# Kernel tuning notes

Measured on AMD Instinct MI355X. Metric: run time of the kernel, lower is better.

The kernel has to match this reference:

```python
import jax, jax.numpy as jnp
import numpy as np

N = 100000      # nodes
E = 3200000     # edges (avg degree 32)
F = 256         # input features
C = 256         # output channels


def setup_inputs() -> dict:
    key = jax.random.key(0)
    k1, k2, k3, k4, k5 = jax.random.split(key, 5)
    x = jax.random.normal(k1, (N, F), dtype=jnp.float32)
    edge_row = jax.random.randint(k2, (E,), 0, N, dtype=jnp.int32)
    edge_col = jax.random.randint(k3, (E,), 0, N, dtype=jnp.int32)
    # precomputed normalized adjacency values (D^-1/2 (A+I) D^-1/2 entries)
    edge_vals = jax.random.uniform(k4, (E,), dtype=jnp.float32)
    kernel = jax.random.normal(k5, (F, C), dtype=jnp.float32) * (1.0 / np.sqrt(F))
    bias = jnp.zeros((C,), dtype=jnp.float32)
    return {"x": x, "edge_row": edge_row, "edge_col": edge_col,
            "edge_vals": edge_vals, "kernel": kernel, "bias": bias}


def reference(x, edge_row, edge_col, edge_vals, kernel, bias):
    # GraphConv: Z = relu( A_hat @ (X @ W) + b ), single mode, sparse A_hat.
    h = x @ kernel                                   # [N, C]
    msgs = edge_vals[:, None] * h[edge_col]          # [E, C] gather along cols
    agg = jax.ops.segment_sum(msgs, edge_row, num_segments=N)  # [N, C]
    return jax.nn.relu(agg + bias)
```

## Files before the change

kernel.cpp:

```cpp
#include <hip/hip_runtime.h>
#include <hip/hip_bf16.h>
#include <hip/hip_fp16.h>


#define BROWS 128
#define CH_A1 16384
#define CH_A3 8192
#define GEMM_SMEM 10240

typedef __attribute__((ext_vector_type(4))) float f32x4;
typedef __attribute__((ext_vector_type(8))) short s16x8;

__device__ __forceinline__ unsigned short f2bf(float f) {
    unsigned u = __float_as_uint(f);
    u += 0x7FFFu + ((u >> 16) & 1u);
    return (unsigned short)(u >> 16);
}
__device__ __forceinline__ float bf2f(unsigned short s) {
    return __uint_as_float(((unsigned)s) << 16);
}

__global__ __launch_bounds__(256) void k_wt(const float* __restrict__ W,
                                            unsigned short* __restrict__ Wt) {
    int idx = blockIdx.x * 256 + threadIdx.x;
    int k = idx >> 8, c = idx & 255;
    Wt[c * 256 + k] = f2bf(W[idx]);
}

__device__ __forceinline__ void gemm_body(const float* __restrict__ X,
                                          const unsigned short* __restrict__ Wt,
                                          unsigned short* __restrict__ H,
                                          int M, int g, char* smem) {
    typedef unsigned short AsRow[40];
    AsRow* As = (AsRow*)smem;
    int t = threadIdx.x;
    int lane = t & 63;
    int w = t >> 6;
    int wm = w & 1, wn = w >> 1;
    int rb = g >> 2, cb4 = g & 3;
    int r0 = rb * 128, c0 = cb4 * 64;

    int srow = t >> 2;
    int sslot = t & 3;
    int gr0 = r0 + srow;        if (gr0 >= M) gr0 = M - 1;
    int gr1 = r0 + 64 + srow;   if (gr1 >= M) gr1 = M - 1;

    f32x4 acc[4][2] = {};

    for (int k0 = 0; k0 < 256; k0 += 32) {
        const float* p0 = &X[(size_t)gr0 * 256 + k0 + sslot * 8];
        const float* p1 = &X[(size_t)gr1 * 256 + k0 + sslot * 8];
        float4 a0 = *(const float4*)p0;
        float4 a1 = *(const float4*)(p0 + 4);
        float4 b0 = *(const float4*)p1;
        float4 b1 = *(const float4*)(p1 + 4);
        s16x8 va, vb;
        va[0] = (short)f2bf(a0.x); va[1] = (short)f2bf(a0.y);
        va[2] = (short)f2bf(a0.z); va[3] = (short)f2bf(a0.w);
        va[4] = (short)f2bf(a1.x); va[5] = (short)f2bf(a1.y);
        va[6] = (short)f2bf(a1.z); va[7] = (short)f2bf(a1.w);
        vb[0] = (short)f2bf(b0.x); vb[1] = (short)f2bf(b0.y);
        vb[2] = (short)f2bf(b0.z); vb[3] = (short)f2bf(b0.w);
        vb[4] = (short)f2bf(b1.x); vb[5] = (short)f2bf(b1.y);
        vb[6] = (short)f2bf(b1.z); vb[7] = (short)f2bf(b1.w);
        __syncthreads();
        *(s16x8*)&As[srow][sslot * 8] = va;
        *(s16x8*)&As[srow + 64][sslot * 8] = vb;
        __syncthreads();

        int kofs = (lane >> 4) * 8;
        s16x8 afr[4], bfr[2];
#pragma unroll
        for (int mi = 0; mi < 4; ++mi)
            afr[mi] = *(const s16x8*)&As[wm * 64 + mi * 16 + (lane & 15)][kofs];
#pragma unroll
        for (int ni = 0; ni < 2; ++ni) {
            int cn = c0 + wn * 32 + ni * 16 + (lane & 15);
            bfr[ni] = *(const s16x8*)&Wt[(size_t)cn * 256 + k0 + kofs];
        }
#pragma unroll
        for (int mi = 0; mi < 4; ++mi)
#pragma unroll
            for (int ni = 0; ni < 2; ++ni)
                acc[mi][ni] = __builtin_amdgcn_mfma_f32_16x16x32_bf16(
                    afr[mi], bfr[ni], acc[mi][ni], 0, 0, 0);
    }

#pragma unroll
    for (int mi = 0; mi < 4; ++mi) {
#pragma unroll
        for (int ni = 0; ni < 2; ++ni) {
            int rg = r0 + wm * 64 + mi * 16 + (lane >> 4) * 4;
            int cg = c0 + wn * 32 + ni * 16 + (lane & 15);
#pragma unroll
            for (int j = 0; j < 4; ++j) {
                if (rg + j < M)
                    H[(size_t)(rg + j) * 256 + cg] = f2bf(acc[mi][ni][j]);
            }
        }
    }
}

__device__ __forceinline__ void hist_body(const int* __restrict__ row,
                                          int* __restrict__ gcnt,
                                          int E, int NB, int chunk, char* smem) {
    int* h = (int*)smem;
    int t = threadIdx.x;
    for (int j = t; j < NB; j += 256) h[j] = 0;
    __syncthreads();
    int start = chunk * CH_A1;
    int end = min(E, start + CH_A1);
    for (int i = start + t; i < end; i += 256)
        atomicAdd(&h[row[i] >> 7], 1);
    __syncthreads();
    for (int j = t; j < NB; j += 256)
        if (h[j]) atomicAdd(&gcnt[j], h[j]);
}

__device__ __forceinline__ void a3_body(const int* __restrict__ row,
                                        const int* __restrict__ col,
                                        const float* __restrict__ val,
                                        int* __restrict__ gcur,
                                        int2* __restrict__ binned,
                                        int E, int NB, int chunk, char* smem) {
    int* h    = (int*)smem;
    int* base = h + NB;
    int* cur  = base + NB;
    int t = threadIdx.x;
    for (int j = t; j < NB; j += 256) { h[j] = 0; cur[j] = 0; }
    __syncthreads();
    int start = chunk * CH_A3;
    int end = min(E, start + CH_A3);
    for (int i = start + t; i < end; i += 256)
        atomicAdd(&h[row[i] >> 7], 1);
    __syncthreads();
    for (int j = t; j < NB; j += 256) {
        int c = h[j];
        base[j] = c ? atomicAdd(&gcur[j], c) : 0;
    }
    __syncthreads();
    for (int i = start + t; i < end; i += 256) {
        int r = row[i];
        int b = r >> 7;
        int ofs = atomicAdd(&cur[b], 1);
        unsigned hb = (unsigned)__half_as_ushort(__float2half(val[i]));
        binned[base[b] + ofs] = make_int2(col[i] | (int)(hb << 17), r & (BROWS - 1));
    }
}

__device__ __forceinline__ void kb_body(const int2* __restrict__ binned,
                                        const int* __restrict__ bkt_base,
                                        int* __restrict__ rowptr,
                                        unsigned* __restrict__ csr,
                                        int N, int b, char* smem) {
    int* cnt = (int*)smem;
    int* sc  = cnt + BROWS;
    int* cur = sc + BROWS;
    int t = threadIdx.x;
    int r0 = b * BROWS;
    int bb = bkt_base[b];
    int be = bkt_base[b + 1];
    if (t < BROWS) cnt[t] = 0;
    __syncthreads();
    for (int i = bb + t; i < be; i += 256)
        atomicAdd(&cnt[binned[i].y], 1);
    __syncthreads();
    if (t < BROWS) sc[t] = cnt[t];
    __syncthreads();
    for (int off = 1; off < BROWS; off <<= 1) {
        int tmp = (t < BROWS && t >= off) ? sc[t - off] : 0;
        __syncthreads();
        if (t < BROWS && t >= off) sc[t] += tmp;
        __syncthreads();
    }
    if (t < BROWS) {
        int ex = sc[t] - cnt[t];
        cur[t] = ex;
        if (r0 + t < N) rowptr[r0 + t] = bb + ex;
    }
    __syncthreads();
    for (int i = bb + t; i < be; i += 256) {
        int2 e = binned[i];
        int ofs = atomicAdd(&cur[e.y], 1);
        csr[bb + ofs] = (unsigned)e.x;
    }
}

__global__ __launch_bounds__(1024) void kA2(const int* __restrict__ gcnt,
                                            int* __restrict__ bkt_base,
                                            int* __restrict__ gcur,
                                            int* __restrict__ rowptr,
                                            int NB, int N, int E) {
    __shared__ int s[1024];
    int t = threadIdx.x;
    int v = (t < NB) ? gcnt[t] : 0;
    s[t] = v;
    __syncthreads();
    for (int off = 1; off < 1024; off <<= 1) {
        int tmp = (t >= off) ? s[t - off] : 0;
        __syncthreads();
        if (t >= off) s[t] += tmp;
        __syncthreads();
    }
    if (t < NB) {
        int ex = s[t] - v;
        bkt_base[t] = ex;
        gcur[t] = ex;
    }
    if (t == 0) {
        bkt_base[NB] = E;
        rowptr[N] = E;
    }
}

__global__ __launch_bounds__(256) void h0(const int* __restrict__ row,
                                          int* __restrict__ gcnt,
                                          int E, int NB, int nHist,
                                          const float* __restrict__ X,
                                          const unsigned short* __restrict__ Wt,
                                          unsigned short* __restrict__ H,
                                          int M, int g0) {
    extern __shared__ char smem[];
    int bid = blockIdx.x;
    if (bid < nHist) { hist_body(row, gcnt, E, NB, bid, smem); return; }
    gemm_body(X, Wt, H, M, g0 + (bid - nHist), smem);
}

__global__ __launch_bounds__(256) void h1(const int* __restrict__ row,
                                          const int* __restrict__ col,
                                          const float* __restrict__ val,
                                          int* __restrict__ gcur,
                                          int2* __restrict__ binned,
                                          int E, int NB, int nA3,
                                          const float* __restrict__ X,
                                          const unsigned short* __restrict__ Wt,
                                          unsigned short* __restrict__ H,
                                          int M, int g0) {
    extern __shared__ char smem[];
    int bid = blockIdx.x;
    if (bid < nA3) { a3_body(row, col, val, gcur, binned, E, NB, bid, smem); return; }
    gemm_body(X, Wt, H, M, g0 + (bid - nA3), smem);
}

__global__ __launch_bounds__(256) void h2(const int2* __restrict__ binned,
                                          const int* __restrict__ bktb,
                                          int* __restrict__ rowptr,
                                          unsigned* __restrict__ csr,
                                          int N, int NB,
                                          const float* __restrict__ X,
                                          const unsigned short* __restrict__ Wt,
                                          unsigned short* __restrict__ H,
                                          int M, int g0) {
    extern __shared__ char smem[];
    int bid = blockIdx.x;
    if (bid < NB) { kb_body(binned, bktb, rowptr, csr, N, bid, smem); return; }
    gemm_body(X, Wt, H, M, g0 + (bid - NB), smem);
}

__global__ __launch_bounds__(256) void k_gemm_solo(const float* __restrict__ X,
                                                   const unsigned short* __restrict__ Wt,
                                                   unsigned short* __restrict__ H, int M) {
    extern __shared__ char smem[];
    gemm_body(X, Wt, H, M, blockIdx.x, smem);
}

__global__ __launch_bounds__(256) void k_agg(const unsigned short* __restrict__ H,
                                             const int* __restrict__ rowptr,
                                             const unsigned* __restrict__ csr,
                                             const float* __restrict__ bias,
                                             float* __restrict__ out, int n) {
    int wave = threadIdx.x >> 6;
    int lane = threadIdx.x & 63;
    int node = blockIdx.x * 4 + wave;
    if (node >= n) return;
    int s = rowptr[node];
    int e = rowptr[node + 1];
    int h = lane >> 5;
    int cbase = (lane & 31) * 8;

    float a0=0.f,a1=0.f,a2=0.f,a3=0.f,a4=0.f,a5=0.f,a6=0.f,a7=0.f;

#define ACC(K, HV)                                                      \
    {                                                                   \
        float v = __half2float(__ushort_as_half((unsigned short)((K) >> 17))); \
        a0 += v * bf2f((unsigned short)(HV)[0]);                        \
        a1 += v * bf2f((unsigned short)(HV)[1]);                        \
        a2 += v * bf2f((unsigned short)(HV)[2]);                        \
        a3 += v * bf2f((unsigned short)(HV)[3]);                        \
        a4 += v * bf2f((unsigned short)(HV)[4]);                        \
        a5 += v * bf2f((unsigned short)(HV)[5]);                        \
        a6 += v * bf2f((unsigned short)(HV)[6]);                        \
        a7 += v * bf2f((unsigned short)(HV)[7]);                        \
    }

    int i = s;
    for (; i + 11 < e; i += 12) {
        unsigned k0 = csr[i + h];
        unsigned k1 = csr[i + 2 + h];
        unsigned k2 = csr[i + 4 + h];
        unsigned k3 = csr[i + 6 + h];
        unsigned k4 = csr[i + 8 + h];
        unsigned k5 = csr[i + 10 + h];
        s16x8 g0 = *(const s16x8*)&H[(k0 & 0x1FFFFu) * 256 + cbase];
        s16x8 g1 = *(const s16x8*)&H[(k1 & 0x1FFFFu) * 256 + cbase];
        s16x8 g2 = *(const s16x8*)&H[(k2 & 0x1FFFFu) * 256 + cbase];
        s16x8 g3 = *(const s16x8*)&H[(k3 & 0x1FFFFu) * 256 + cbase];
        s16x8 g4 = *(const s16x8*)&H[(k4 & 0x1FFFFu) * 256 + cbase];
        s16x8 g5 = *(const s16x8*)&H[(k5 & 0x1FFFFu) * 256 + cbase];
        ACC(k0, g0); ACC(k1, g1); ACC(k2, g2);
        ACC(k3, g3); ACC(k4, g4); ACC(k5, g5);
    }
    for (; i + 3 < e; i += 4) {
        unsigned k0 = csr[i + h];
        unsigned k1 = csr[i + 2 + h];
        s16x8 g0 = *(const s16x8*)&H[(k0 & 0x1FFFFu) * 256 + cbase];
        s16x8 g1 = *(const s16x8*)&H[(k1 & 0x1FFFFu) * 256 + cbase];
        ACC(k0, g0); ACC(k1, g1);
    }
    for (; i + 1 < e; i += 2) {
        unsigned k0 = csr[i + h];
        s16x8 g0 = *(const s16x8*)&H[(k0 & 0x1FFFFu) * 256 + cbase];
        ACC(k0, g0);
    }
    if (i < e) {
        unsigned k0 = csr[i];
        s16x8 g0 = *(const s16x8*)&H[(k0 & 0x1FFFFu) * 256 + cbase];
        float v = h ? 0.f
                    : __half2float(__ushort_as_half((unsigned short)(k0 >> 17)));
        a0 += v * bf2f((unsigned short)g0[0]);
        a1 += v * bf2f((unsigned short)g0[1]);
        a2 += v * bf2f((unsigned short)g0[2]);
        a3 += v * bf2f((unsigned short)g0[3]);
        a4 += v * bf2f((unsigned short)g0[4]);
        a5 += v * bf2f((unsigned short)g0[5]);
        a6 += v * bf2f((unsigned short)g0[6]);
        a7 += v * bf2f((unsigned short)g0[7]);
    }
#undef ACC

    a0 += __shfl_xor(a0, 32); a1 += __shfl_xor(a1, 32);
    a2 += __shfl_xor(a2, 32); a3 += __shfl_xor(a3, 32);
    a4 += __shfl_xor(a4, 32); a5 += __shfl_xor(a5, 32);
    a6 += __shfl_xor(a6, 32); a7 += __shfl_xor(a7, 32);

    float w0 = h ? a4 : a0;
    float w1 = h ? a5 : a1;
    float w2 = h ? a6 : a2;
    float w3 = h ? a7 : a3;
    int cw = cbase + h * 4;
    float4 b4 = *(const float4*)&bias[cw];
    float4 o;
    o.x = fmaxf(w0 + b4.x, 0.f);
    o.y = fmaxf(w1 + b4.y, 0.f);
    o.z = fmaxf(w2 + b4.z, 0.f);
    o.w = fmaxf(w3 + b4.w, 0.f);
    *(float4*)&out[node * 256 + cw] = o;
}

extern "C" void kernel_launch(void* const* d_in, const int* in_sizes, int n_in,
                              void* d_out, int out_size, void* d_ws, size_t ws_size,
                              hipStream_t stream) {
    const float* x     = (const float*)d_in[0];
    const int*   erow  = (const int*)d_in[1];
    const int*   ecol  = (const int*)d_in[2];
    const float* evals = (const float*)d_in[3];
    const float* W     = (const float*)d_in[4];
    const float* bias  = (const float*)d_in[5];
    float* out = (float*)d_out;

    const int C = 256;
    const int N = in_sizes[0] / C;
    const int E = in_sizes[1];
    const int NB = (N + BROWS - 1) / BROWS;

    char* ws = (char*)d_ws;
    size_t off = 0;
    auto carve = [&](size_t bytes) -> void* {
        void* p = ws + off;
        off += (bytes + 255) & ~(size_t)255;
        return p;
    };
    unsigned short* Hbf  = (unsigned short*)carve((size_t)N * C * 2);
    unsigned*       csr  = (unsigned*)carve((size_t)E * 4);
    int*            rowp = (int*)carve((size_t)(N + 1) * 4);
    unsigned short* Wt   = (unsigned short*)carve((size_t)C * 256 * 2);
    int*            gcnt = (int*)carve((size_t)NB * 4);
    int*            gcur = (int*)carve((size_t)NB * 4);
    int*            bktb = (int*)carve((size_t)(NB + 1) * 4);

    bool fused = (off + (size_t)E * 8) <= ws_size;
    int2* binned = fused ? (int2*)carve((size_t)E * 8) : (int2*)Hbf;

    int nHist = (E + CH_A1 - 1) / CH_A1;
    int nA3   = (E + CH_A3 - 1) / CH_A3;
    int gemmBlocks = ((N + 127) / 128) * 4;

    int G0 = fused ? 600 : 0;
    int G1 = fused ? 1400 : 0;
    int G2 = fused ? (gemmBlocks - 600 - 1400) : 0;

    hipMemsetAsync(gcnt, 0, (size_t)NB * 4, stream);
    k_wt<<<256, 256, 0, stream>>>(W, Wt);
    h0<<<nHist + G0, 256, GEMM_SMEM, stream>>>(erow, gcnt, E, NB, nHist,
                                               x, Wt, Hbf, N, 0);
    kA2<<<1, 1024, 0, stream>>>(gcnt, bktb, gcur, rowp, NB, N, E);
    h1<<<nA3 + G1, 256, GEMM_SMEM, stream>>>(erow, ecol, evals, gcur, binned,
                                             E, NB, nA3, x, Wt, Hbf, N, G0);
    h2<<<NB + G2, 256, GEMM_SMEM, stream>>>(binned, bktb, rowp, csr, N, NB,
                                            x, Wt, Hbf, N, G0 + G1);
    if (!fused)
        k_gemm_solo<<<gemmBlocks, 256, GEMM_SMEM, stream>>>(x, Wt, Hbf, N);

    k_agg<<<(N + 3) / 4, 256, 0, stream>>>(Hbf, rowp, csr, bias, out, N);
}
```

Before: 432.0 us.

## Retile GEMM to 64x256 blocks, fold weight transpose into histogram launch, use nontemporal accesses

The GEMM block tile changes from 128x64 to 64 rows by all 256 columns, so each X row is loaded and converted to bf16 once instead of four times. The weight transpose moves into the histogram kernel h0, and the GEMM blocks are redistributed across h1 and h2 only. Nontemporal loads and stores are added for X, the binned edges and the output. The aggregation unroll drops from 12 to 8 edges per iteration. The trade-off is more accumulator registers per wave and a different overlap balance between graph preprocessing and the GEMM.

```diff
diff --git a/kernel.cpp b/kernel.cpp
--- a/kernel.cpp
+++ b/kernel.cpp
@@ -9,6 +9,7 @@
 #define GEMM_SMEM 10240
 
 typedef __attribute__((ext_vector_type(4))) float f32x4;
+typedef __attribute__((ext_vector_type(2))) int i32x2;
 typedef __attribute__((ext_vector_type(8))) short s16x8;
 
 __device__ __forceinline__ unsigned short f2bf(float f) {
@@ -18,13 +19,6 @@
 }
 __device__ __forceinline__ float bf2f(unsigned short s) {
     return __uint_as_float(((unsigned)s) << 16);
-}
-
-__global__ __launch_bounds__(256) void k_wt(const float* __restrict__ W,
-                                            unsigned short* __restrict__ Wt) {
-    int idx = blockIdx.x * 256 + threadIdx.x;
-    int k = idx >> 8, c = idx & 255;
-    Wt[c * 256 + k] = f2bf(W[idx]);
 }
 
 __device__ __forceinline__ void gemm_body(const float* __restrict__ X,
@@ -36,52 +30,41 @@
     int t = threadIdx.x;
     int lane = t & 63;
     int w = t >> 6;
-    int wm = w & 1, wn = w >> 1;
-    int rb = g >> 2, cb4 = g & 3;
-    int r0 = rb * 128, c0 = cb4 * 64;
-
+    int r0 = g * 64;
+    int c0 = w * 64;
     int srow = t >> 2;
     int sslot = t & 3;
-    int gr0 = r0 + srow;        if (gr0 >= M) gr0 = M - 1;
-    int gr1 = r0 + 64 + srow;   if (gr1 >= M) gr1 = M - 1;
-
-    f32x4 acc[4][2] = {};
+    int gr = r0 + srow; if (gr >= M) gr = M - 1;
+
+    f32x4 acc[4][4] = {};
 
     for (int k0 = 0; k0 < 256; k0 += 32) {
-        const float* p0 = &X[(size_t)gr0 * 256 + k0 + sslot * 8];
-        const float* p1 = &X[(size_t)gr1 * 256 + k0 + sslot * 8];
-        float4 a0 = *(const float4*)p0;
-        float4 a1 = *(const float4*)(p0 + 4);
-        float4 b0 = *(const float4*)p1;
-        float4 b1 = *(const float4*)(p1 + 4);
-        s16x8 va, vb;
-        va[0] = (short)f2bf(a0.x); va[1] = (short)f2bf(a0.y);
-        va[2] = (short)f2bf(a0.z); va[3] = (short)f2bf(a0.w);
-        va[4] = (short)f2bf(a1.x); va[5] = (short)f2bf(a1.y);
-        va[6] = (short)f2bf(a1.z); va[7] = (short)f2bf(a1.w);
-        vb[0] = (short)f2bf(b0.x); vb[1] = (short)f2bf(b0.y);
-        vb[2] = (short)f2bf(b0.z); vb[3] = (short)f2bf(b0.w);
-        vb[4] = (short)f2bf(b1.x); vb[5] = (short)f2bf(b1.y);
-        vb[6] = (short)f2bf(b1.z); vb[7] = (short)f2bf(b1.w);
+        const float* p = &X[(size_t)gr * 256 + k0 + sslot * 8];
+        f32x4 a0 = __builtin_nontemporal_load((const f32x4*)p);
+        f32x4 a1 = __builtin_nontemporal_load((const f32x4*)(p + 4));
+        s16x8 va;
+        va[0] = (short)f2bf(a0[0]); va[1] = (short)f2bf(a0[1]);
+        va[2] = (short)f2bf(a0[2]); va[3] = (short)f2bf(a0[3]);
+        va[4] = (short)f2bf(a1[0]); va[5] = (short)f2bf(a1[1]);
+        va[6] = (short)f2bf(a1[2]); va[7] = (short)f2bf(a1[3]);
         __syncthreads();
         *(s16x8*)&As[srow][sslot * 8] = va;
-        *(s16x8*)&As[srow + 64][sslot * 8] = vb;
         __syncthreads();
 
         int kofs = (lane >> 4) * 8;
-        s16x8 afr[4], bfr[2];
+        s16x8 afr[4], bfr[4];
 #pragma unroll
         for (int mi = 0; mi < 4; ++mi)
-            afr[mi] = *(const s16x8*)&As[wm * 64 + mi * 16 + (lane & 15)][kofs];
-#pragma unroll
-        for (int ni = 0; ni < 2; ++ni) {
-            int cn = c0 + wn * 32 + ni * 16 + (lane & 15);
+            afr[mi] = *(const s16x8*)&As[mi * 16 + (lane & 15)][kofs];
+#pragma unroll
+        for (int ni = 0; ni < 4; ++ni) {
+            int cn = c0 + ni * 16 + (lane & 15);
             bfr[ni] = *(const s16x8*)&Wt[(size_t)cn * 256 + k0 + kofs];
         }
 #pragma unroll
         for (int mi = 0; mi < 4; ++mi)
 #pragma unroll
-            for (int ni = 0; ni < 2; ++ni)
+            for (int ni = 0; ni < 4; ++ni)
                 acc[mi][ni] = __builtin_amdgcn_mfma_f32_16x16x32_bf16(
                     afr[mi], bfr[ni], acc[mi][ni], 0, 0, 0);
     }
@@ -89,9 +72,9 @@
 #pragma unroll
     for (int mi = 0; mi < 4; ++mi) {
 #pragma unroll
-        for (int ni = 0; ni < 2; ++ni) {
-            int rg = r0 + wm * 64 + mi * 16 + (lane >> 4) * 4;
-            int cg = c0 + wn * 32 + ni * 16 + (lane & 15);
+        for (int ni = 0; ni < 4; ++ni) {
+            int rg = r0 + mi * 16 + (lane >> 4) * 4;
+            int cg = c0 + ni * 16 + (lane & 15);
 #pragma unroll
             for (int j = 0; j < 4; ++j) {
                 if (rg + j < M)
@@ -162,8 +145,10 @@
     int be = bkt_base[b + 1];
     if (t < BROWS) cnt[t] = 0;
     __syncthreads();
-    for (int i = bb + t; i < be; i += 256)
-        atomicAdd(&cnt[binned[i].y], 1);
+    for (int i = bb + t; i < be; i += 256) {
+        i32x2 e = __builtin_nontemporal_load((const i32x2*)&binned[i]);
+        atomicAdd(&cnt[e[1]], 1);
+    }
     __syncthreads();
     if (t < BROWS) sc[t] = cnt[t];
     __syncthreads();
@@ -180,9 +165,9 @@
     }
     __syncthreads();
     for (int i = bb + t; i < be; i += 256) {
-        int2 e = binned[i];
-        int ofs = atomicAdd(&cur[e.y], 1);
-        csr[bb + ofs] = (unsigned)e.x;
+        i32x2 e = __builtin_nontemporal_load((const i32x2*)&binned[i]);
+        int ofs = atomicAdd(&cur[e[1]], 1);
+        csr[bb + ofs] = (unsigned)e[0];
     }
 }
 
@@ -216,14 +201,15 @@
 __global__ __launch_bounds__(256) void h0(const int* __restrict__ row,
                                           int* __restrict__ gcnt,
                                           int E, int NB, int nHist,
-                                          const float* __restrict__ X,
-                                          const unsigned short* __restrict__ Wt,
-                                          unsigned short* __restrict__ H,
-                                          int M, int g0) {
+                                          const float* __restrict__ W,
+                                          unsigned short* __restrict__ Wt) {
     extern __shared__ char smem[];
     int bid = blockIdx.x;
+    int t = threadIdx.x;
     if (bid < nHist) { hist_body(row, gcnt, E, NB, bid, smem); return; }
-    gemm_body(X, Wt, H, M, g0 + (bid - nHist), smem);
+    int idx = (bid - nHist) * 256 + t;
+    int k = idx >> 8, c = idx & 255;
+    Wt[c * 256 + k] = f2bf(W[idx]);
 }
 
 __global__ __launch_bounds__(256) void h1(const int* __restrict__ row,
@@ -294,28 +280,16 @@
     }
 
     int i = s;
-    for (; i + 11 < e; i += 12) {
+    for (; i + 7 < e; i += 8) {
         unsigned k0 = csr[i + h];
         unsigned k1 = csr[i + 2 + h];
         unsigned k2 = csr[i + 4 + h];
         unsigned k3 = csr[i + 6 + h];
-        unsigned k4 = csr[i + 8 + h];
-        unsigned k5 = csr[i + 10 + h];
         s16x8 g0 = *(const s16x8*)&H[(k0 & 0x1FFFFu) * 256 + cbase];
         s16x8 g1 = *(const s16x8*)&H[(k1 & 0x1FFFFu) * 256 + cbase];
         s16x8 g2 = *(const s16x8*)&H[(k2 & 0x1FFFFu) * 256 + cbase];
         s16x8 g3 = *(const s16x8*)&H[(k3 & 0x1FFFFu) * 256 + cbase];
-        s16x8 g4 = *(const s16x8*)&H[(k4 & 0x1FFFFu) * 256 + cbase];
-        s16x8 g5 = *(const s16x8*)&H[(k5 & 0x1FFFFu) * 256 + cbase];
-        ACC(k0, g0); ACC(k1, g1); ACC(k2, g2);
-        ACC(k3, g3); ACC(k4, g4); ACC(k5, g5);
-    }
-    for (; i + 3 < e; i += 4) {
-        unsigned k0 = csr[i + h];
-        unsigned k1 = csr[i + 2 + h];
-        s16x8 g0 = *(const s16x8*)&H[(k0 & 0x1FFFFu) * 256 + cbase];
-        s16x8 g1 = *(const s16x8*)&H[(k1 & 0x1FFFFu) * 256 + cbase];
-        ACC(k0, g0); ACC(k1, g1);
+        ACC(k0, g0); ACC(k1, g1); ACC(k2, g2); ACC(k3, g3);
     }
     for (; i + 1 < e; i += 2) {
         unsigned k0 = csr[i + h];
@@ -349,12 +323,12 @@
     float w3 = h ? a7 : a3;
     int cw = cbase + h * 4;
     float4 b4 = *(const float4*)&bias[cw];
-    float4 o;
-    o.x = fmaxf(w0 + b4.x, 0.f);
-    o.y = fmaxf(w1 + b4.y, 0.f);
-    o.z = fmaxf(w2 + b4.z, 0.f);
-    o.w = fmaxf(w3 + b4.w, 0.f);
-    *(float4*)&out[node * 256 + cw] = o;
+    f32x4 o;
+    o[0] = fmaxf(w0 + b4.x, 0.f);
+    o[1] = fmaxf(w1 + b4.y, 0.f);
+    o[2] = fmaxf(w2 + b4.z, 0.f);
+    o[3] = fmaxf(w3 + b4.w, 0.f);
+    __builtin_nontemporal_store(o, (f32x4*)&out[node * 256 + cw]);
 }
 
 extern "C" void kernel_launch(void* const* d_in, const int* in_sizes, int n_in,
@@ -393,21 +367,18 @@
 
     int nHist = (E + CH_A1 - 1) / CH_A1;
     int nA3   = (E + CH_A3 - 1) / CH_A3;
-    int gemmBlocks = ((N + 127) / 128) * 4;
-
-    int G0 = fused ? 600 : 0;
-    int G1 = fused ? 1400 : 0;
-    int G2 = fused ? (gemmBlocks - 600 - 1400) : 0;
+    int gemmBlocks = (N + 63) / 64;
+
+    int G1 = fused ? 650 : 0;
+    int G2 = fused ? (gemmBlocks - 650) : 0;
 
     hipMemsetAsync(gcnt, 0, (size_t)NB * 4, stream);
-    k_wt<<<256, 256, 0, stream>>>(W, Wt);
-    h0<<<nHist + G0, 256, GEMM_SMEM, stream>>>(erow, gcnt, E, NB, nHist,
-                                               x, Wt, Hbf, N, 0);
+    h0<<<nHist + 256, 256, GEMM_SMEM, stream>>>(erow, gcnt, E, NB, nHist, W, Wt);
     kA2<<<1, 1024, 0, stream>>>(gcnt, bktb, gcur, rowp, NB, N, E);
     h1<<<nA3 + G1, 256, GEMM_SMEM, stream>>>(erow, ecol, evals, gcur, binned,
-                                             E, NB, nA3, x, Wt, Hbf, N, G0);
+                                             E, NB, nA3, x, Wt, Hbf, N, 0);
     h2<<<NB + G2, 256, GEMM_SMEM, stream>>>(binned, bktb, rowp, csr, N, NB,
-                                            x, Wt, Hbf, N, G0 + G1);
+                                            x, Wt, Hbf, N, G1);
     if (!fused)
         k_gemm_solo<<<gemmBlocks, 256, GEMM_SMEM, stream>>>(x, Wt, Hbf, N);
 
```

New measurement: 396.9 us. -8.1%, faster.
